# Kernel optimization log

Measured on AMD Instinct MI355X. Metric: run time of the kernel, lower is better.

The kernel has to match this reference:

```python
import jax, jax.numpy as jnp
import numpy as np


def setup_inputs() -> dict:
    key = jax.random.key(0)
    ks = jax.random.split(key, 5)
    N, D, H, E = 8192, 1024, 4096, 8
    s = 0.02
    return {
        "x": jax.random.normal(ks[0], (N, D), jnp.float32),
        "Wr": jax.random.normal(ks[1], (D, E), jnp.float32) * s,
        "br": jnp.zeros((E,), jnp.float32),
        "W1": jax.random.normal(ks[2], (E, D, H), jnp.float32) * s,
        "b1": jnp.zeros((E, H), jnp.float32),
        "W2": jax.random.normal(ks[3], (E, H, D), jnp.float32) * s,
        "b2": jnp.zeros((E, D), jnp.float32),
        "k": 2,
    }


def reference(x, Wr, br, W1, b1, W2, b2, k):
    # Router (eval mode: no gate noise)
    logits = x @ Wr + br                      # [N, E]
    scores = jax.nn.softmax(logits, axis=-1)  # [N, E]
    topk_vals, topk_inds = jax.lax.top_k(scores, k)  # [N, k]
    N, E = scores.shape
    # dispatch_mask: zeros scattered with top-k probabilities
    dispatch_mask = jnp.zeros_like(scores).at[
        jnp.arange(N)[:, None], topk_inds
    ].set(topk_vals)                          # [N, E]
    # Dense all-expert FFN compute (faithful to the original wasteful pattern)
    h = jax.nn.relu(jnp.einsum('nd,edh->neh', x, W1) + b1)   # [N, E, H]
    expert_outputs = jnp.einsum('neh,ehd->ned', h, W2) + b2  # [N, E, D]
    output = jnp.einsum('ned,ne->nd', expert_outputs, dispatch_mask)  # [N, D]
    # Load-balancing aux loss (torch.var is unbiased, ddof=1)
    importance = dispatch_mask.sum(axis=0)    # [E]
    imp_mean = jnp.mean(importance)
    imp_var = jnp.var(importance, ddof=1)
    aux_loss = imp_var / (imp_mean ** 2 + 1e-9)
    return output, aux_loss
```

## Files before the change

kernel.cpp:

```cpp
#include <hip/hip_runtime.h>
#include <hip/hip_bf16.h>


#define NTOK 8192
#define DDIM 1024
#define HDIM 4096
#define NEXP 8
#define NASSIGN (NTOK * 2)
#define MAX_MT 135
#define GRID1 (32 * MAX_MT)
#define GRID2 (8 * 4 * MAX_MT)

typedef __bf16 bf16_t;
typedef __bf16 bf16x2 __attribute__((ext_vector_type(2)));
typedef __bf16 bf16x4 __attribute__((ext_vector_type(4)));
typedef __bf16 bf16x8 __attribute__((ext_vector_type(8)));
typedef float f32x4 __attribute__((ext_vector_type(4)));

#define GLOAD16(gptr, lptr)                                                    \
  __builtin_amdgcn_global_load_lds(                                            \
      (const __attribute__((address_space(1))) void*)(gptr),                   \
      (__attribute__((address_space(3))) void*)(lptr), 16, 0, 0)

#define VMCNT(n) asm volatile("s_waitcnt vmcnt(" #n ")" ::: "memory")

__device__ __forceinline__ int xcd_swz(int orig, int nwg) {
  const int cpx = nwg >> 3;
  return (orig & 7) * cpx + (orig >> 3);
}

__global__ void __launch_bounds__(256) transpose_cvt_kernel(
    const float* __restrict__ in, bf16_t* __restrict__ out, int R, int C) {
  __shared__ float tile[64][33];
  const size_t mat = (size_t)R * C;
  const float* ip = in + (size_t)blockIdx.z * mat;
  bf16_t* op = out + (size_t)blockIdx.z * mat;
  const int c0 = blockIdx.x * 32, r0 = blockIdx.y * 64;
  const int tx = threadIdx.x, ty = threadIdx.y;
#pragma unroll
  for (int i = 0; i < 8; ++i) {
    const int r = ty + 8 * i;
    tile[r][tx] = ip[(size_t)(r0 + r) * C + (c0 + tx)];
  }
  __syncthreads();
#pragma unroll
  for (int j = 0; j < 4; ++j) {
    const int c = ty + 8 * j;
    bf16x2 v;
    v[0] = (bf16_t)tile[2 * tx][c];
    v[1] = (bf16_t)tile[2 * tx + 1][c];
    *(bf16x2*)(op + (size_t)(c0 + c) * R + r0 + 2 * tx) = v;
  }
}

__global__ void __launch_bounds__(256) router_kernel(
    const float* __restrict__ x, const float* __restrict__ Wr,
    const float* __restrict__ br, int2* __restrict__ ids,
    float2* __restrict__ prs, int* __restrict__ counts,
    bf16_t* __restrict__ xb) {
  const int n = blockIdx.x;
  const int t = threadIdx.x;
  const int wave = t >> 6, lane = t & 63;
  const float4 xv = ((const float4*)(x + (size_t)n * DDIM))[t];
  bf16x4 o;
  o[0] = (bf16_t)xv.x; o[1] = (bf16_t)xv.y;
  o[2] = (bf16_t)xv.z; o[3] = (bf16_t)xv.w;
  ((bf16x4*)(xb + (size_t)n * DDIM))[t] = o;

  float acc[NEXP];
#pragma unroll
  for (int e = 0; e < NEXP; ++e) acc[e] = 0.f;
  const float xq[4] = {xv.x, xv.y, xv.z, xv.w};
#pragma unroll
  for (int q = 0; q < 4; ++q) {
    const float* w = Wr + (size_t)(4 * t + q) * NEXP;
#pragma unroll
    for (int e = 0; e < NEXP; ++e) acc[e] += xq[q] * w[e];
  }
#pragma unroll
  for (int off = 32; off >= 1; off >>= 1)
#pragma unroll
    for (int e = 0; e < NEXP; ++e) acc[e] += __shfl_down(acc[e], off);
  __shared__ float red[4][NEXP];
  if (lane == 0)
#pragma unroll
    for (int e = 0; e < NEXP; ++e) red[wave][e] = acc[e];
  __syncthreads();
  if (t == 0) {
    float l[NEXP];
#pragma unroll
    for (int e = 0; e < NEXP; ++e)
      l[e] = ((red[0][e] + red[1][e]) + (red[2][e] + red[3][e])) + br[e];
    int i1 = 0; float v1 = l[0];
    for (int e = 1; e < NEXP; ++e)
      if (l[e] > v1) { v1 = l[e]; i1 = e; }
    int i2 = (i1 == 0) ? 1 : 0; float v2 = l[i2];
    for (int e = 0; e < NEXP; ++e)
      if (e != i1 && l[e] > v2) { v2 = l[e]; i2 = e; }
    float denom = 0.f;
    for (int e = 0; e < NEXP; ++e) denom += expf(l[e] - v1);
    ids[n] = make_int2(i1, i2);
    prs[n] = make_float2(1.f / denom, expf(v2 - v1) / denom);
    atomicAdd(&counts[i1], 1);
    atomicAdd(&counts[i2], 1);
  }
}

__global__ void __launch_bounds__(256) scan_aux_kernel(
    const int* __restrict__ counts, int* __restrict__ offsets,
    int* __restrict__ tmap, const int2* __restrict__ ids,
    const float2* __restrict__ prs, float* __restrict__ aux_out) {
  const int t = threadIdx.x;
  if (t == 0) {
    int off = 0, nt = 0;
    for (int e = 0; e < NEXP; ++e) {
      offsets[e] = off;
      const int c = counts[e];
      for (int m0 = 0; m0 < c; m0 += 128) {
        tmap[nt] = e;
        tmap[MAX_MT + nt] = m0;
        ++nt;
      }
      off += c;
    }
    offsets[NEXP] = off;
    tmap[2 * MAX_MT] = nt;
  }
  float imp[NEXP];
#pragma unroll
  for (int e = 0; e < NEXP; ++e) imp[e] = 0.f;
  for (int n = t; n < NTOK; n += 256) {
    const int2 id = ids[n];
    const float2 pr = prs[n];
#pragma unroll
    for (int e = 0; e < NEXP; ++e)
      imp[e] += (id.x == e ? pr.x : 0.f) + (id.y == e ? pr.y : 0.f);
  }
  __shared__ float red[256][NEXP];
#pragma unroll
  for (int e = 0; e < NEXP; ++e) red[t][e] = imp[e];
  __syncthreads();
  for (int s = 128; s >= 1; s >>= 1) {
    if (t < s) {
#pragma unroll
      for (int e = 0; e < NEXP; ++e) red[t][e] += red[t + s][e];
    }
    __syncthreads();
  }
  if (t == 0) {
    float m = 0.f;
    for (int e = 0; e < NEXP; ++e) m += red[0][e];
    m *= (1.f / NEXP);
    float v = 0.f;
    for (int e = 0; e < NEXP; ++e) {
      const float d = red[0][e] - m;
      v += d * d;
    }
    v *= (1.f / (NEXP - 1));
    aux_out[0] = v / (m * m + 1e-9f);
  }
}

__global__ void __launch_bounds__(256) scatter_kernel(
    const int2* __restrict__ ids, const float2* __restrict__ prs,
    const int* __restrict__ offsets, int* __restrict__ cursor,
    int* __restrict__ btok, float* __restrict__ bprob) {
  const int n = blockIdx.x * 256 + threadIdx.x;
  if (n >= NTOK) return;
  const int2 id = ids[n];
  const float2 pr = prs[n];
  int p = atomicAdd(&cursor[id.x], 1);
  btok[offsets[id.x] + p] = n;
  bprob[offsets[id.x] + p] = pr.x;
  p = atomicAdd(&cursor[id.y], 1);
  btok[offsets[id.y] + p] = n;
  bprob[offsets[id.y] + p] = pr.y;
}


__global__ void __launch_bounds__(256, 3) gemm1_kernel(
    const bf16_t* __restrict__ xb, const bf16_t* __restrict__ W1t,
    const float* __restrict__ b1, const int* __restrict__ btok,
    const int* __restrict__ offsets, const int* __restrict__ counts,
    const int* __restrict__ tmap, bf16_t* __restrict__ h) {
  const int job = xcd_swz((int)blockIdx.x, GRID1);
  const int tidx = job >> 5;
  const int nblk = job & 31;
  if (tidx >= tmap[2 * MAX_MT]) return;
  const int e = tmap[tidx];
  const int m0 = tmap[MAX_MT + tidx];
  const int cnt = counts[e];
  const int aoff = offsets[e];
  const int n0 = nblk * 128;

  __shared__ __align__(16) bf16_t Al[3][128 * 32];
  __shared__ __align__(16) bf16_t Bl[3][128 * 32];

  const int tid = threadIdx.x;
  const int wave = tid >> 6;
  const int lane = tid & 63;

  const bf16_t* asrc[2];
  const bf16_t* bsrc[2];
#pragma unroll
  for (int j = 0; j < 2; ++j) {
    const int c = j * 256 + tid;
    const int r = c >> 2;
    const int slot = (c & 3) ^ ((r >> 1) & 3);
    int arow = m0 + r;
    if (arow > cnt - 1) arow = cnt - 1;
    asrc[j] = xb + (size_t)btok[aoff + arow] * DDIM + slot * 8;
    bsrc[j] = W1t + ((size_t)e * HDIM + n0 + r) * DDIM + slot * 8;
  }

  const int wr = (wave >> 1) * 64;
  const int wc = (wave & 1) * 64;
  const int lrow = lane & 15;
  const int lslot = lane >> 4;

  int aoffb[4], boffb[4];
#pragma unroll
  for (int f = 0; f < 4; ++f) {
    const int Rr = wr + f * 16 + lrow;
    aoffb[f] = Rr * 64 + ((lslot ^ ((Rr >> 1) & 3)) << 4);
    const int Cc = wc + f * 16 + lrow;
    boffb[f] = Cc * 64 + ((lslot ^ ((Cc >> 1) & 3)) << 4);
  }

  f32x4 acc[4][4];
#pragma unroll
  for (int mf = 0; mf < 4; ++mf)
#pragma unroll
    for (int nf = 0; nf < 4; ++nf) acc[mf][nf] = (f32x4){0.f, 0.f, 0.f, 0.f};

  auto stage = [&](int b, int t) {
    char* Ab = (char*)&Al[b][0] + wave * 1024;
    char* Bb = (char*)&Bl[b][0] + wave * 1024;
    const int ko = t * 32;
#pragma unroll
    for (int j = 0; j < 2; ++j) {
      GLOAD16(asrc[j] + ko, Ab + j * 4096);
      GLOAD16(bsrc[j] + ko, Bb + j * 4096);
    }
  };
  auto compute = [&](int b) {
    const char* Ab = (const char*)&Al[b][0];
    const char* Bb = (const char*)&Bl[b][0];
    bf16x8 af[4], bfr[4];
#pragma unroll
    for (int f = 0; f < 4; ++f) {
      af[f] = *(const bf16x8*)(Ab + aoffb[f]);
      bfr[f] = *(const bf16x8*)(Bb + boffb[f]);
    }
    __builtin_amdgcn_s_setprio(1);
#pragma unroll
    for (int mf = 0; mf < 4; ++mf)
#pragma unroll
      for (int nf = 0; nf < 4; ++nf)
        acc[mf][nf] = __builtin_amdgcn_mfma_f32_16x16x32_bf16(
            af[mf], bfr[nf], acc[mf][nf], 0, 0, 0);
    __builtin_amdgcn_s_setprio(0);
  };

  stage(0, 0);
  stage(1, 1);
  int cb = 0, pb = 2;
  for (int t = 0; t < 31; ++t) {
    VMCNT(4);
    __builtin_amdgcn_s_barrier();
    __builtin_amdgcn_sched_barrier(0);
    if (t + 2 < 32) stage(pb, t + 2);
    compute(cb);
    cb = (cb == 2) ? 0 : cb + 1;
    pb = (pb == 2) ? 0 : pb + 1;
  }
  VMCNT(0);
  __builtin_amdgcn_s_barrier();
  __builtin_amdgcn_sched_barrier(0);
  compute(cb);

  const int rbase = (lane >> 4) * 4;
  const float* b1e = b1 + (size_t)e * HDIM + n0;
#pragma unroll
  for (int nf = 0; nf < 4; ++nf) {
    const int cl = wc + nf * 16 + lrow;
    const float bb = b1e[cl];
#pragma unroll
    for (int mf = 0; mf < 4; ++mf) {
#pragma unroll
      for (int r = 0; r < 4; ++r) {
        const int grow = wr + mf * 16 + rbase + r;
        if (m0 + grow < cnt)
          h[(size_t)(aoff + m0 + grow) * HDIM + (n0 + cl)] =
              (bf16_t)fmaxf(acc[mf][nf][r] + bb, 0.f);
      }
    }
  }
}

__global__ void __launch_bounds__(256, 3) gemm2_kernel(
    const bf16_t* __restrict__ h, const bf16_t* __restrict__ W2t,
    const float* __restrict__ b2, const int* __restrict__ btok,
    const float* __restrict__ bprob, const int* __restrict__ offsets,
    const int* __restrict__ counts, const int* __restrict__ tmap,
    float* __restrict__ out) {
  const int job = xcd_swz((int)blockIdx.x, GRID2);
  const int tidx = job >> 5;
  const int nblk = job & 7;
  const int kch = (job >> 3) & 3;
  if (tidx >= tmap[2 * MAX_MT]) return;
  const int e = tmap[tidx];
  const int m0 = tmap[MAX_MT + tidx];
  const int cnt = counts[e];
  const int aoff = offsets[e];
  const int n0 = nblk * 128;

  __shared__ __align__(16) bf16_t Al[3][128 * 32];
  __shared__ __align__(16) bf16_t Bl[3][128 * 32];

  const int tid = threadIdx.x;
  const int wave = tid >> 6;
  const int lane = tid & 63;

  const bf16_t* asrc[2];
  const bf16_t* bsrc[2];
#pragma unroll
  for (int j = 0; j < 2; ++j) {
    const int c = j * 256 + tid;
    const int r = c >> 2;
    const int slot = (c & 3) ^ ((r >> 1) & 3);
    int arow = m0 + r;
    if (arow > cnt - 1) arow = cnt - 1;
    asrc[j] = h + (size_t)(aoff + arow) * HDIM + kch * 1024 + slot * 8;
    bsrc[j] = W2t + ((size_t)e * DDIM + n0 + r) * HDIM + kch * 1024 + slot * 8;
  }

  const int wr = (wave >> 1) * 64;
  const int wc = (wave & 1) * 64;
  const int lrow = lane & 15;
  const int lslot = lane >> 4;

  int aoffb[4], boffb[4];
#pragma unroll
  for (int f = 0; f < 4; ++f) {
    const int Rr = wr + f * 16 + lrow;
    aoffb[f] = Rr * 64 + ((lslot ^ ((Rr >> 1) & 3)) << 4);
    const int Cc = wc + f * 16 + lrow;
    boffb[f] = Cc * 64 + ((lslot ^ ((Cc >> 1) & 3)) << 4);
  }

  f32x4 acc[4][4];
#pragma unroll
  for (int mf = 0; mf < 4; ++mf)
#pragma unroll
    for (int nf = 0; nf < 4; ++nf) acc[mf][nf] = (f32x4){0.f, 0.f, 0.f, 0.f};

  auto stage = [&](int b, int t) {
    char* Ab = (char*)&Al[b][0] + wave * 1024;
    char* Bb = (char*)&Bl[b][0] + wave * 1024;
    const int ko = t * 32;
#pragma unroll
    for (int j = 0; j < 2; ++j) {
      GLOAD16(asrc[j] + ko, Ab + j * 4096);
      GLOAD16(bsrc[j] + ko, Bb + j * 4096);
    }
  };
  auto compute = [&](int b) {
    const char* Ab = (const char*)&Al[b][0];
    const char* Bb = (const char*)&Bl[b][0];
    bf16x8 af[4], bfr[4];
#pragma unroll
    for (int f = 0; f < 4; ++f) {
      af[f] = *(const bf16x8*)(Ab + aoffb[f]);
      bfr[f] = *(const bf16x8*)(Bb + boffb[f]);
    }
    __builtin_amdgcn_s_setprio(1);
#pragma unroll
    for (int mf = 0; mf < 4; ++mf)
#pragma unroll
      for (int nf = 0; nf < 4; ++nf)
        acc[mf][nf] = __builtin_amdgcn_mfma_f32_16x16x32_bf16(
            af[mf], bfr[nf], acc[mf][nf], 0, 0, 0);
    __builtin_amdgcn_s_setprio(0);
  };

  stage(0, 0);
  stage(1, 1);
  int cb = 0, pb = 2;
  for (int t = 0; t < 31; ++t) {
    VMCNT(4);
    __builtin_amdgcn_s_barrier();
    __builtin_amdgcn_sched_barrier(0);
    if (t + 2 < 32) stage(pb, t + 2);
    compute(cb);
    cb = (cb == 2) ? 0 : cb + 1;
    pb = (pb == 2) ? 0 : pb + 1;
  }
  VMCNT(0);
  __builtin_amdgcn_s_barrier();
  __builtin_amdgcn_sched_barrier(0);
  compute(cb);

  const int rbase = (lane >> 4) * 4;
  const float* b2e = b2 + (size_t)e * DDIM + n0;
  float bb[4];
#pragma unroll
  for (int nf = 0; nf < 4; ++nf)
    bb[nf] = (kch == 0) ? b2e[wc + nf * 16 + lrow] : 0.f;
#pragma unroll
  for (int mf = 0; mf < 4; ++mf) {
#pragma unroll
    for (int r = 0; r < 4; ++r) {
      const int grow = wr + mf * 16 + rbase + r;
      if (m0 + grow < cnt) {
        const int assign = aoff + m0 + grow;
        const int tok = btok[assign];
        const float p = bprob[assign];
        float* orow = out + (size_t)tok * DDIM + n0;
#pragma unroll
        for (int nf = 0; nf < 4; ++nf) {
          const int cl = wc + nf * 16 + lrow;
          atomicAdd(&orow[cl], (acc[mf][nf][r] + bb[nf]) * p);
        }
      }
    }
  }
}


extern "C" void kernel_launch(void* const* d_in, const int* in_sizes, int n_in,
                              void* d_out, int out_size, void* d_ws,
                              size_t ws_size, hipStream_t stream) {
  const float* x = (const float*)d_in[0];
  const float* Wr = (const float*)d_in[1];
  const float* br = (const float*)d_in[2];
  const float* W1 = (const float*)d_in[3];
  const float* b1 = (const float*)d_in[4];
  const float* W2 = (const float*)d_in[5];
  const float* b2 = (const float*)d_in[6];

  char* w = (char*)d_ws;
  auto alloc = [&](size_t bytes) -> char* {
    char* p = w;
    w += (bytes + 255) & ~(size_t)255;
    return p;
  };
  bf16_t* xb = (bf16_t*)alloc((size_t)NTOK * DDIM * 2);
  bf16_t* W1t = (bf16_t*)alloc((size_t)NEXP * DDIM * HDIM * 2);
  bf16_t* W2t = (bf16_t*)alloc((size_t)NEXP * DDIM * HDIM * 2);
  bf16_t* hbuf = (bf16_t*)alloc((size_t)NASSIGN * HDIM * 2);
  int* btok = (int*)alloc(NASSIGN * 4);
  float* bprob = (float*)alloc(NASSIGN * 4);
  int2* ids = (int2*)alloc(NTOK * 8);
  float2* prs = (float2*)alloc(NTOK * 8);
  int* ctrl = (int*)alloc(64);
  int* offsets = (int*)alloc(64);
  int* tmap = (int*)alloc((2 * MAX_MT + 1) * 4);
  int* counts = ctrl;
  int* cursor = ctrl + 8;
  (void)in_sizes; (void)n_in; (void)ws_size;

  float* out = (float*)d_out;

  hipMemsetAsync(d_out, 0, (size_t)out_size * 4, stream);
  hipMemsetAsync(ctrl, 0, 64, stream);

  transpose_cvt_kernel<<<dim3(HDIM / 32, DDIM / 64, NEXP), dim3(32, 8), 0,
                         stream>>>(W1, W1t, DDIM, HDIM);
  transpose_cvt_kernel<<<dim3(DDIM / 32, HDIM / 64, NEXP), dim3(32, 8), 0,
                         stream>>>(W2, W2t, HDIM, DDIM);
  router_kernel<<<NTOK, 256, 0, stream>>>(x, Wr, br, ids, prs, counts, xb);
  scan_aux_kernel<<<1, 256, 0, stream>>>(counts, offsets, tmap, ids, prs,
                                         out + (size_t)NTOK * DDIM);
  scatter_kernel<<<NTOK / 256, 256, 0, stream>>>(ids, prs, offsets, cursor,
                                                 btok, bprob);
  gemm1_kernel<<<GRID1, 256, 0, stream>>>(xb, W1t, b1, btok, offsets, counts,
                                          tmap, hbuf);
  gemm2_kernel<<<GRID2, 256, 0, stream>>>(hbuf, W2t, b2, btok, bprob, offsets,
                                          counts, tmap, out);
}
```

Measured before the change: 941.3 us.

## Replace gemm2 atomic scatter-add with split-K buffer writes and a combine kernel

The second GEMM no longer scatters results with fp32 atomicAdd into the output. It now splits K two ways, not four, writes plain per-assignment partial outputs into two workspace buffers, and a new combine kernel gathers each token's two assignments and applies the routing weights. This also removes the output memset. The cost is extra memory traffic, since 128MB of partials are written and read back. The second buffer reuses the start of the workspace, overwriting xb and W1t after gemm1 has finished with them. Scheduling barriers are also relaxed to mask 0x1, and an atomic fallback path is kept for when the workspace is too small.

```diff
diff --git a/kernel.cpp b/kernel.cpp
--- a/kernel.cpp
+++ b/kernel.cpp
@@ -9,7 +9,8 @@
 #define NASSIGN (NTOK * 2)
 #define MAX_MT 135
 #define GRID1 (32 * MAX_MT)
-#define GRID2 (8 * 4 * MAX_MT)
+#define GRID2A (8 * 2 * MAX_MT)
+#define GRID2B (8 * MAX_MT)
 
 typedef __bf16 bf16_t;
 typedef __bf16 bf16x2 __attribute__((ext_vector_type(2)));
@@ -164,17 +165,41 @@
 __global__ void __launch_bounds__(256) scatter_kernel(
     const int2* __restrict__ ids, const float2* __restrict__ prs,
     const int* __restrict__ offsets, int* __restrict__ cursor,
-    int* __restrict__ btok, float* __restrict__ bprob) {
+    int* __restrict__ btok, float* __restrict__ bprob,
+    int2* __restrict__ amap) {
   const int n = blockIdx.x * 256 + threadIdx.x;
   if (n >= NTOK) return;
   const int2 id = ids[n];
   const float2 pr = prs[n];
   int p = atomicAdd(&cursor[id.x], 1);
-  btok[offsets[id.x] + p] = n;
-  bprob[offsets[id.x] + p] = pr.x;
+  const int a1 = offsets[id.x] + p;
+  btok[a1] = n;
+  bprob[a1] = pr.x;
   p = atomicAdd(&cursor[id.y], 1);
-  btok[offsets[id.y] + p] = n;
-  bprob[offsets[id.y] + p] = pr.y;
+  const int a2 = offsets[id.y] + p;
+  btok[a2] = n;
+  bprob[a2] = pr.y;
+  amap[n] = make_int2(a1, a2);
+}
+
+__global__ void __launch_bounds__(256) combine_kernel(
+    const float* __restrict__ o0, const float* __restrict__ o1,
+    const int2* __restrict__ amap, const float* __restrict__ bprob,
+    float* __restrict__ out) {
+  const int n = blockIdx.x;
+  const int d = threadIdx.x * 4;
+  const int2 a = amap[n];
+  const float p1 = bprob[a.x], p2 = bprob[a.y];
+  const float4 u0 = *(const float4*)(o0 + (size_t)a.x * DDIM + d);
+  const float4 u1 = *(const float4*)(o1 + (size_t)a.x * DDIM + d);
+  const float4 v0 = *(const float4*)(o0 + (size_t)a.y * DDIM + d);
+  const float4 v1 = *(const float4*)(o1 + (size_t)a.y * DDIM + d);
+  float4 r;
+  r.x = p1 * (u0.x + u1.x) + p2 * (v0.x + v1.x);
+  r.y = p1 * (u0.y + u1.y) + p2 * (v0.y + v1.y);
+  r.z = p1 * (u0.z + u1.z) + p2 * (v0.z + v1.z);
+  r.w = p1 * (u0.w + u1.w) + p2 * (v0.w + v1.w);
+  *(float4*)(out + (size_t)n * DDIM + d) = r;
 }
 
 
@@ -268,7 +293,7 @@
   for (int t = 0; t < 31; ++t) {
     VMCNT(4);
     __builtin_amdgcn_s_barrier();
-    __builtin_amdgcn_sched_barrier(0);
+    __builtin_amdgcn_sched_barrier(0x1);
     if (t + 2 < 32) stage(pb, t + 2);
     compute(cb);
     cb = (cb == 2) ? 0 : cb + 1;
@@ -276,7 +301,7 @@
   }
   VMCNT(0);
   __builtin_amdgcn_s_barrier();
-  __builtin_amdgcn_sched_barrier(0);
+  __builtin_amdgcn_sched_barrier(0x1);
   compute(cb);
 
   const int rbase = (lane >> 4) * 4;
@@ -298,22 +323,27 @@
   }
 }
 
+template <int NT, int KSP, bool ATOMIC>
 __global__ void __launch_bounds__(256, 3) gemm2_kernel(
     const bf16_t* __restrict__ h, const bf16_t* __restrict__ W2t,
     const float* __restrict__ b2, const int* __restrict__ btok,
     const float* __restrict__ bprob, const int* __restrict__ offsets,
     const int* __restrict__ counts, const int* __restrict__ tmap,
+    float* __restrict__ o0, float* __restrict__ o1,
     float* __restrict__ out) {
-  const int job = xcd_swz((int)blockIdx.x, GRID2);
-  const int tidx = job >> 5;
-  const int nblk = job & 7;
-  const int kch = (job >> 3) & 3;
+  const int nwg = 8 * KSP * MAX_MT;
+  const int job = xcd_swz((int)blockIdx.x, nwg);
+  const int tidx = job / (8 * KSP);
+  const int rem = job % (8 * KSP);
+  const int nblk = rem & 7;
+  const int kch = rem >> 3;
   if (tidx >= tmap[2 * MAX_MT]) return;
   const int e = tmap[tidx];
   const int m0 = tmap[MAX_MT + tidx];
   const int cnt = counts[e];
   const int aoff = offsets[e];
   const int n0 = nblk * 128;
+  const int kbase = kch * (HDIM / KSP);
 
   __shared__ __align__(16) bf16_t Al[3][128 * 32];
   __shared__ __align__(16) bf16_t Bl[3][128 * 32];
@@ -331,8 +361,8 @@
     const int slot = (c & 3) ^ ((r >> 1) & 3);
     int arow = m0 + r;
     if (arow > cnt - 1) arow = cnt - 1;
-    asrc[j] = h + (size_t)(aoff + arow) * HDIM + kch * 1024 + slot * 8;
-    bsrc[j] = W2t + ((size_t)e * DDIM + n0 + r) * HDIM + kch * 1024 + slot * 8;
+    asrc[j] = h + (size_t)(aoff + arow) * HDIM + kbase + slot * 8;
+    bsrc[j] = W2t + ((size_t)e * DDIM + n0 + r) * HDIM + kbase + slot * 8;
   }
 
   const int wr = (wave >> 1) * 64;
@@ -387,18 +417,18 @@
   stage(0, 0);
   stage(1, 1);
   int cb = 0, pb = 2;
-  for (int t = 0; t < 31; ++t) {
+  for (int t = 0; t < NT - 1; ++t) {
     VMCNT(4);
     __builtin_amdgcn_s_barrier();
-    __builtin_amdgcn_sched_barrier(0);
-    if (t + 2 < 32) stage(pb, t + 2);
+    __builtin_amdgcn_sched_barrier(0x1);
+    if (t + 2 < NT) stage(pb, t + 2);
     compute(cb);
     cb = (cb == 2) ? 0 : cb + 1;
     pb = (pb == 2) ? 0 : pb + 1;
   }
   VMCNT(0);
   __builtin_amdgcn_s_barrier();
-  __builtin_amdgcn_sched_barrier(0);
+  __builtin_amdgcn_sched_barrier(0x1);
   compute(cb);
 
   const int rbase = (lane >> 4) * 4;
@@ -407,20 +437,41 @@
 #pragma unroll
   for (int nf = 0; nf < 4; ++nf)
     bb[nf] = (kch == 0) ? b2e[wc + nf * 16 + lrow] : 0.f;
-#pragma unroll
-  for (int mf = 0; mf < 4; ++mf) {
-#pragma unroll
-    for (int r = 0; r < 4; ++r) {
-      const int grow = wr + mf * 16 + rbase + r;
-      if (m0 + grow < cnt) {
-        const int assign = aoff + m0 + grow;
-        const int tok = btok[assign];
-        const float p = bprob[assign];
-        float* orow = out + (size_t)tok * DDIM + n0;
-#pragma unroll
-        for (int nf = 0; nf < 4; ++nf) {
-          const int cl = wc + nf * 16 + lrow;
-          atomicAdd(&orow[cl], (acc[mf][nf][r] + bb[nf]) * p);
+
+  if (ATOMIC) {
+#pragma unroll
+    for (int mf = 0; mf < 4; ++mf) {
+#pragma unroll
+      for (int r = 0; r < 4; ++r) {
+        const int grow = wr + mf * 16 + rbase + r;
+        if (m0 + grow < cnt) {
+          const int assign = aoff + m0 + grow;
+          const int tok = btok[assign];
+          const float p = bprob[assign];
+          float* orow = out + (size_t)tok * DDIM + n0;
+#pragma unroll
+          for (int nf = 0; nf < 4; ++nf) {
+            const int cl = wc + nf * 16 + lrow;
+            atomicAdd(&orow[cl], (acc[mf][nf][r] + bb[nf]) * p);
+          }
+        }
+      }
+    }
+  } else {
+    float* obase = (kch == 0) ? o0 : o1;
+#pragma unroll
+    for (int mf = 0; mf < 4; ++mf) {
+#pragma unroll
+      for (int r = 0; r < 4; ++r) {
+        const int grow = wr + mf * 16 + rbase + r;
+        if (m0 + grow < cnt) {
+          const int assign = aoff + m0 + grow;
+          float* orow = obase + (size_t)assign * DDIM + n0;
+#pragma unroll
+          for (int nf = 0; nf < 4; ++nf) {
+            const int cl = wc + nf * 16 + lrow;
+            orow[cl] = acc[mf][nf][r] + bb[nf];
+          }
         }
       }
     }
@@ -453,17 +504,24 @@
   float* bprob = (float*)alloc(NASSIGN * 4);
   int2* ids = (int2*)alloc(NTOK * 8);
   float2* prs = (float2*)alloc(NTOK * 8);
+  int2* amap = (int2*)alloc(NTOK * 8);
   int* ctrl = (int*)alloc(64);
   int* offsets = (int*)alloc(64);
   int* tmap = (int*)alloc((2 * MAX_MT + 1) * 4);
   int* counts = ctrl;
   int* cursor = ctrl + 8;
-  (void)in_sizes; (void)n_in; (void)ws_size;
+  const size_t osz = (size_t)NASSIGN * DDIM * 4;
+  float* o0 = (float*)alloc(osz);
+  float* o1 = (float*)d_ws;
+  const size_t needed = (size_t)(w - (char*)d_ws);
+  const bool pathA = ws_size >= needed;
+  (void)in_sizes; (void)n_in;
 
   float* out = (float*)d_out;
 
-  hipMemsetAsync(d_out, 0, (size_t)out_size * 4, stream);
   hipMemsetAsync(ctrl, 0, 64, stream);
+  if (!pathA)
+    hipMemsetAsync(d_out, 0, (size_t)out_size * 4, stream);
 
   transpose_cvt_kernel<<<dim3(HDIM / 32, DDIM / 64, NEXP), dim3(32, 8), 0,
                          stream>>>(W1, W1t, DDIM, HDIM);
@@ -473,9 +531,15 @@
   scan_aux_kernel<<<1, 256, 0, stream>>>(counts, offsets, tmap, ids, prs,
                                          out + (size_t)NTOK * DDIM);
   scatter_kernel<<<NTOK / 256, 256, 0, stream>>>(ids, prs, offsets, cursor,
-                                                 btok, bprob);
+                                                 btok, bprob, amap);
   gemm1_kernel<<<GRID1, 256, 0, stream>>>(xb, W1t, b1, btok, offsets, counts,
                                           tmap, hbuf);
-  gemm2_kernel<<<GRID2, 256, 0, stream>>>(hbuf, W2t, b2, btok, bprob, offsets,
-                                          counts, tmap, out);
-}
+  if (pathA) {
+    gemm2_kernel<64, 2, false><<<GRID2A, 256, 0, stream>>>(
+        hbuf, W2t, b2, btok, bprob, offsets, counts, tmap, o0, o1, out);
+    combine_kernel<<<NTOK, 256, 0, stream>>>(o0, o1, amap, bprob, out);
+  } else {
+    gemm2_kernel<128, 1, true><<<GRID2B, 256, 0, stream>>>(
+        hbuf, W2t, b2, btok, bprob, offsets, counts, tmap, o0, o1, out);
+  }
+}
```

After: 816.5 us. -13.3%, faster.
